# Optimization experiments

Hardware: AMD Instinct MI355X
Metric: run time of the kernel (lower is better)

The kernel has to match this reference:

```python
import jax, jax.numpy as jnp
import numpy as np
from jax import lax
from jax.scipy.special import logsumexp

B, T, N = 256, 512, 128


def setup_inputs() -> dict:
    key = jax.random.key(0)
    k1, k2, k3 = jax.random.split(key, 3)
    emissions = jax.random.normal(k1, (B, T, N), dtype=jnp.float32)
    tag_ids = jax.random.randint(k2, (B, T), 0, N, dtype=jnp.int64)
    mask = jnp.ones((B, T), dtype=jnp.int32)
    # learned transition matrix (glorot-uniform-ish init)
    limit = float(np.sqrt(6.0 / (N + N)))
    trans = jax.random.uniform(k3, (N, N), minval=-limit, maxval=limit, dtype=jnp.float32)
    return {"emissions": emissions, "tag_ids": tag_ids, "mask": mask, "trans": trans}


def _sequence_score(emissions, tag_ids, maskf, trans):
    # unary: emission score of the gold tag at each valid step
    unary = jnp.take_along_axis(emissions, tag_ids[:, :, None], axis=2)[..., 0]  # [B,T]
    unary = jnp.sum(unary * maskf, axis=1)
    # binary: transition score between consecutive gold tags
    binary = trans[tag_ids[:, :-1], tag_ids[:, 1:]] * maskf[:, 1:]  # [B,T-1]
    return unary + jnp.sum(binary, axis=1)


def _log_norm(emissions, maskf, trans):
    # forward algorithm over time via lax.scan; alpha: [B,N]
    alpha0 = emissions[:, 0]
    em = jnp.swapaxes(emissions, 0, 1)[1:]   # [T-1,B,N]
    mk = jnp.swapaxes(maskf, 0, 1)[1:]       # [T-1,B]

    def step(alpha, xs):
        emit_t, m_t = xs
        new = logsumexp(alpha[:, :, None] + trans[None], axis=1) + emit_t
        alpha = jnp.where(m_t[:, None] > 0, new, alpha)
        return alpha, None

    alpha, _ = lax.scan(step, alpha0, (em, mk))
    return logsumexp(alpha, axis=1)  # [B]


def _viterbi_decode(emissions, maskf, trans):
    alpha0 = emissions[:, 0]
    em = jnp.swapaxes(emissions, 0, 1)[1:]
    mk = jnp.swapaxes(maskf, 0, 1)[1:]
    idx = jnp.arange(N, dtype=jnp.int32)[None]

    def fwd(alpha, xs):
        emit_t, m_t = xs
        scores = alpha[:, :, None] + trans[None]        # [B,N,N]
        bp = jnp.argmax(scores, axis=1).astype(jnp.int32)  # [B,N]
        new = jnp.max(scores, axis=1) + emit_t
        valid = m_t[:, None] > 0
        alpha = jnp.where(valid, new, alpha)
        bp = jnp.where(valid, bp, idx)  # carry same tag through padding
        return alpha, bp

    alpha, bps = lax.scan(fwd, alpha0, (em, mk))  # bps: [T-1,B,N]
    last_tag = jnp.argmax(alpha, axis=1).astype(jnp.int32)  # [B]

    def bwd(tag, bp_t):
        new_tag = jnp.take_along_axis(bp_t, tag[:, None], axis=1)[:, 0]
        return new_tag, new_tag

    _, tags_rev = lax.scan(bwd, last_tag, bps[::-1])  # [T-1,B]
    tags = jnp.concatenate([tags_rev[::-1], last_tag[None]], axis=0)  # [T,B]
    return jnp.swapaxes(tags, 0, 1)  # [B,T]


def reference(emissions, tag_ids, mask, trans):
    maskf = mask.astype(emissions.dtype)
    log_likelihood = _sequence_score(emissions, tag_ids, maskf, trans) - _log_norm(emissions, maskf, trans)
    predict = _viterbi_decode(emissions, maskf, trans)
    return (log_likelihood, trans, predict)
```

## Files before the change

kernel.cpp:

```cpp
#include <hip/hip_runtime.h>
#include <cmath>

#define BB 256
#define TT 512
#define NN 128
#define LN2F 0.6931471805599453f

typedef __bf16 bf16x8 __attribute__((ext_vector_type(8)));
typedef float floatx4 __attribute__((ext_vector_type(4)));

__device__ __forceinline__ float wave_max64(float v) {
    #pragma unroll
    for (int off = 32; off; off >>= 1) v = fmaxf(v, __shfl_xor(v, off));
    return v;
}
__device__ __forceinline__ float wave_sum64(float v) {
    #pragma unroll
    for (int off = 32; off; off >>= 1) v += __shfl_xor(v, off);
    return v;
}
__device__ __forceinline__ int wave_argmax128(float v0, float v1, int l) {
    float m = fmaxf(v0, v1);
    float wm = wave_max64(m);
    unsigned long long ball = __ballot(m == wm);
    int lane = __ffsll(ball) - 1;
    int idx = (v0 == wm) ? (2 * l) : (2 * l + 1);
    return __shfl(idx, lane);
}

__device__ __forceinline__ __bf16 to_bf16(float f) {
    unsigned u = __float_as_uint(f);
    unsigned r = (u + 0x7FFFu + ((u >> 16) & 1u)) >> 16;
    union { unsigned short s; __bf16 b; } cv;
    cv.s = (unsigned short)r;
    return cv.b;
}

__device__ __forceinline__ int padidx16(int i) { return 20 * (i >> 4) + (i & 15); }

__global__ __launch_bounds__(1024, 4) void fused_kernel(
        const float* __restrict__ em, const int* __restrict__ gtags,
        const int* __restrict__ mask, const float* __restrict__ trans,
        float* __restrict__ out_ll, float* __restrict__ out_trans,
        float* __restrict__ outp) {
    const int b = blockIdx.x;
    const int tid = threadIdx.x;
    const int w = tid >> 6;
    const int l = tid & 63;
    const int jv = (l & 7) + 8 * w;
    const int q = l >> 3;
    const int i0 = 16 * q;
    const bool sAct = (w < 8);
    const int js = (l & 15) + 16 * (w & 7);
    const int qs = l >> 4;

    __shared__ __align__(16) float stA[1440], stB[1440];
    __shared__ __align__(16) __bf16 sbf[2][NN];
    __shared__ unsigned char bp_lds[TT * NN];
    __shared__ unsigned char tags_lds[TT];
    __shared__ unsigned char map_lds[16 * NN];
    __shared__ int entry_sh[16];
    __shared__ int msk[TT];
    __shared__ float piv[2];
    __shared__ float sfin[NN];
    __shared__ float wsum[16];
    __shared__ float llnorm_sh;
    __shared__ int misc[2];

    if (tid < TT) msk[tid] = mask[b * TT + tid];

    const float* emb = em + (size_t)b * TT * NN;

    float C[16];
    {
        const float* tc = trans + (size_t)i0 * NN + jv;
        #pragma unroll
        for (int r = 0; r < 16; ++r) C[r] = tc[(size_t)r * NN];
    }
    float st;
    {
        float a0 = emb[jv];
        st = a0;
        if (l < 8) stA[padidx16(jv)] = a0;
    }
    float e_next = emb[NN + jv];

    bf16x8 Bf[4];
    float ss = 0.f, es_next = 0.f;
    int kacc = 0;
    if (sAct) {
        #pragma unroll
        for (int kc = 0; kc < 4; ++kc) {
            #pragma unroll
            for (int jj = 0; jj < 8; ++jj) {
                int row = kc * 32 + qs * 8 + jj;
                Bf[kc][jj] = to_bf16(__expf(trans[(size_t)row * NN + js]));
            }
        }
        ss = __expf(emb[js]);
        if (l < 16) sbf[0][js] = to_bf16(ss);
        if (tid == 0) piv[0] = ss;
        es_next = emb[NN + js];
    }
    __syncthreads();

    const float4* apA = (const float4*)(stA + 20 * q);
    const float4* apB = (const float4*)(stB + 20 * q);

    auto STEP = [&](int t, const float4* ap, float* dst) {
        const float e_cur = e_next;
        const float es_cur = es_next;
        if (t + 1 < TT) {
            e_next = emb[(size_t)(t + 1) * NN + jv];
            if (sAct) es_next = emb[(size_t)(t + 1) * NN + js];
        }
        const int m = msk[t];
        float m0 = -INFINITY, m1 = -INFINITY, m2 = -INFINITY, m3 = -INFINITY;
        int u0 = 0, u1 = 0, u2 = 0, u3 = 0;
        #pragma unroll
        for (int u = 0; u < 4; ++u) {
            float4 v = ap[u];
            float c0 = v.x + C[4*u+0]; u0 = (c0 > m0) ? u : u0; m0 = fmaxf(m0, c0);
            float c1 = v.y + C[4*u+1]; u1 = (c1 > m1) ? u : u1; m1 = fmaxf(m1, c1);
            float c2 = v.z + C[4*u+2]; u2 = (c2 > m2) ? u : u2; m2 = fmaxf(m2, c2);
            float c3 = v.w + C[4*u+3]; u3 = (c3 > m3) ? u : u3; m3 = fmaxf(m3, c3);
        }
        float bv = m0; int bx = i0 + 4 * u0;
        { int id = i0 + 4*u1 + 1; if (m1 > bv || (m1 == bv && id < bx)) { bv = m1; bx = id; } }
        { int id = i0 + 4*u2 + 2; if (m2 > bv || (m2 == bv && id < bx)) { bv = m2; bx = id; } }
        { int id = i0 + 4*u3 + 3; if (m3 > bv || (m3 == bv && id < bx)) { bv = m3; bx = id; } }
        #pragma unroll
        for (int off = 8; off <= 32; off <<= 1) {
            float ov = __shfl_xor(bv, off);
            int oi = __shfl_xor(bx, off);
            if (ov > bv || (ov == bv && oi < bx)) { bv = ov; bx = oi; }
        }
        if (l < 8) {
            float an; int bp;
            if (m) { an = bv + e_cur; bp = bx; }
            else   { an = st;         bp = jv; }
            st = an;
            dst[padidx16(jv)] = an;
            bp_lds[t * NN + jv] = (unsigned char)bp;
        }
        if (sAct) {
            if (m) {
                const int p = (t - 1) & 1;
                const __bf16* sp = sbf[p];
                floatx4 acc = {0.f, 0.f, 0.f, 0.f};
                #pragma unroll
                for (int kc = 0; kc < 4; ++kc) {
                    bf16x8 a = *(const bf16x8*)(sp + kc * 32 + qs * 8);
                    acc = __builtin_amdgcn_mfma_f32_16x16x32_bf16(a, Bf[kc], acc, 0, 0, 0);
                }
                float dot = acc[0];
                const float pv = piv[p];
                const int k = (int)(__float_as_uint(pv) >> 23) - 127;
                const float scale = __uint_as_float((unsigned)(127 - k) << 23);
                ss = dot * scale * __expf(es_cur);
                if (tid == 0) kacc += k;
            }
            const int qb = t & 1;
            if (l < 16) sbf[qb][js] = to_bf16(ss);
            if (tid == 0) piv[qb] = ss;
        }
        __syncthreads();
    };

    for (int t = 1; t < TT - 1; t += 2) {
        STEP(t, apA, stB);
        STEP(t + 1, apB, stA);
    }
    STEP(TT - 1, apA, stB);

    if (sAct && l < 16) sfin[js] = ss;
    if (tid == 0) misc[1] = kacc;
    if (w == 0) {
        float a0 = stB[padidx16(2 * l)], a1 = stB[padidx16(2 * l + 1)];
        int tg = wave_argmax128(a0, a1, l);
        if (l == 0) { misc[0] = tg; tags_lds[TT - 1] = (unsigned char)tg; }
    }
    if (tid < 64) out_trans[b * 64 + tid] = trans[b * 64 + tid];
    __syncthreads();
    if (w == 1) {
        float v = sfin[2 * l] + sfin[2 * l + 1];
        v = wave_sum64(v);
        if (l == 0) llnorm_sh = __logf(v) + (float)misc[1] * LN2F;
    }
    const int lo = 32 * w + 1;
    const int hi = (w == 15) ? (TT - 1) : (32 * w + 32);
    {
        int tA = 2 * l, tB = 2 * l + 1;
        for (int t = hi; t >= lo; --t) {
            tA = bp_lds[t * NN + tA];
            tB = bp_lds[t * NN + tB];
        }
        map_lds[w * NN + 2 * l]     = (unsigned char)tA;
        map_lds[w * NN + 2 * l + 1] = (unsigned char)tB;
    }
    __syncthreads();
    if (tid == 0) {
        int e = misc[0];
        entry_sh[15] = e;
        for (int c = 15; c >= 1; --c) { e = map_lds[c * NN + e]; entry_sh[c - 1] = e; }
    }
    __syncthreads();
    if (l == 0) {
        int tg = entry_sh[w];
        for (int t = hi; t >= lo; --t) {
            tg = bp_lds[t * NN + tg];
            tags_lds[t - 1] = (unsigned char)tg;
        }
    }
    __syncthreads();
    float acc = 0.f;
    if (tid < TT) {
        outp[(size_t)b * TT + tid] = (float)tags_lds[tid];
        int tg = gtags[b * TT + tid];
        float mf = (float)msk[tid];
        acc = emb[(size_t)tid * NN + tg] * mf;
        if (tid >= 1) {
            int tp = gtags[b * TT + tid - 1];
            acc += trans[tp * NN + tg] * mf;
        }
    }
    acc = wave_sum64(acc);
    if (l == 0) wsum[w] = acc;
    __syncthreads();
    if (tid == 0) {
        float s = 0.f;
        #pragma unroll
        for (int i = 0; i < 16; ++i) s += wsum[i];
        out_ll[b] = s - llnorm_sh;
    }
}

extern "C" void kernel_launch(void* const* d_in, const int* in_sizes, int n_in,
                              void* d_out, int out_size, void* d_ws, size_t ws_size,
                              hipStream_t stream) {
    const float* em = (const float*)d_in[0];
    const int* gtags = (const int*)d_in[1];
    const int* mask = (const int*)d_in[2];
    const float* trans = (const float*)d_in[3];

    float* out = (float*)d_out;
    float* out_ll = out;
    float* out_trans = out + BB;
    float* out_pred = out + BB + NN * NN;

    hipLaunchKernelGGL(fused_kernel, dim3(BB), dim3(1024), 0, stream,
                       em, gtags, mask, trans, out_ll, out_trans, out_pred);
}
```

Before: 623.5 us.

## Split Viterbi and forward recurrences into separate blocks

The single fused per-batch block is split into two kinds of blocks, launched as a 2x-sized grid. The first half runs the Viterbi max-plus recurrence and backtrace, and the second half runs the MFMA-based forward log-sum-exp recurrence plus the gold-sequence score. Each block's per-step critical path and barrier work shrink, and the two chains for a sequence can run concurrently on different CUs or co-reside on one. In exchange, each block still reserves the full static shared memory, the forward block leaves half its waves idle at barriers, and emissions are read twice.

```diff
diff --git a/kernel.cpp b/kernel.cpp
--- a/kernel.cpp
+++ b/kernel.cpp
@@ -38,23 +38,19 @@
 
 __device__ __forceinline__ int padidx16(int i) { return 20 * (i >> 4) + (i & 15); }
 
-__global__ __launch_bounds__(1024, 4) void fused_kernel(
+__global__ __launch_bounds__(1024, 8) void fwd_kernel(
         const float* __restrict__ em, const int* __restrict__ gtags,
         const int* __restrict__ mask, const float* __restrict__ trans,
         float* __restrict__ out_ll, float* __restrict__ out_trans,
         float* __restrict__ outp) {
-    const int b = blockIdx.x;
+    const int bi = blockIdx.x;
+    const bool isV = bi < BB;
+    const int b = isV ? bi : bi - BB;
     const int tid = threadIdx.x;
     const int w = tid >> 6;
     const int l = tid & 63;
-    const int jv = (l & 7) + 8 * w;
-    const int q = l >> 3;
-    const int i0 = 16 * q;
-    const bool sAct = (w < 8);
-    const int js = (l & 15) + 16 * (w & 7);
-    const int qs = l >> 4;
-
-    __shared__ __align__(16) float stA[1440], stB[1440];
+
+    __shared__ __align__(16) float stA[160], stB[160];
     __shared__ __align__(16) __bf16 sbf[2][NN];
     __shared__ unsigned char bp_lds[TT * NN];
     __shared__ unsigned char tags_lds[TT];
@@ -63,7 +59,7 @@
     __shared__ int msk[TT];
     __shared__ float piv[2];
     __shared__ float sfin[NN];
-    __shared__ float wsum[16];
+    __shared__ float wsum[8];
     __shared__ float llnorm_sh;
     __shared__ int misc[2];
 
@@ -71,167 +67,182 @@
 
     const float* emb = em + (size_t)b * TT * NN;
 
-    float C[16];
-    {
-        const float* tc = trans + (size_t)i0 * NN + jv;
-        #pragma unroll
-        for (int r = 0; r < 16; ++r) C[r] = tc[(size_t)r * NN];
-    }
-    float st;
-    {
-        float a0 = emb[jv];
-        st = a0;
-        if (l < 8) stA[padidx16(jv)] = a0;
-    }
-    float e_next = emb[NN + jv];
-
-    bf16x8 Bf[4];
-    float ss = 0.f, es_next = 0.f;
-    int kacc = 0;
-    if (sAct) {
-        #pragma unroll
-        for (int kc = 0; kc < 4; ++kc) {
+    if (isV) {
+        const int jv = (l & 7) + 8 * w;
+        const int q = l >> 3;
+        const int i0 = 16 * q;
+        float4 c0, c1, c2, c3;
+        {
+            const float* tc = trans + (size_t)i0 * NN + jv;
+            #define LDC(cc, u) cc.x = tc[(4*u+0)*NN]; cc.y = tc[(4*u+1)*NN]; \
+                               cc.z = tc[(4*u+2)*NN]; cc.w = tc[(4*u+3)*NN];
+            LDC(c0, 0) LDC(c1, 1) LDC(c2, 2) LDC(c3, 3)
+            #undef LDC
+        }
+        float st;
+        {
+            float a0 = emb[jv];
+            st = a0;
+            if (l < 8) stA[padidx16(jv)] = a0;
+        }
+        float e_next = emb[NN + jv];
+        __syncthreads();
+
+        const float4* apA = (const float4*)(stA + 20 * q);
+        const float4* apB = (const float4*)(stB + 20 * q);
+
+        auto VSTEP = [&](int t, const float4* ap, float* dst) {
+            const float e_cur = e_next;
+            if (t + 1 < TT) e_next = emb[(size_t)(t + 1) * NN + jv];
+            const int m = msk[t];
+            float4 v0 = ap[0], v1 = ap[1], v2 = ap[2], v3 = ap[3];
+            float m0 = -INFINITY, m1 = -INFINITY, m2 = -INFINITY, m3 = -INFINITY;
+            int u0 = 0, u1 = 0, u2 = 0, u3 = 0;
+            #define CH(vv, cc, u) { \
+                float a = vv.x + cc.x; u0 = (a > m0) ? u : u0; m0 = fmaxf(m0, a); \
+                float bq = vv.y + cc.y; u1 = (bq > m1) ? u : u1; m1 = fmaxf(m1, bq); \
+                float c = vv.z + cc.z; u2 = (c > m2) ? u : u2; m2 = fmaxf(m2, c); \
+                float d = vv.w + cc.w; u3 = (d > m3) ? u : u3; m3 = fmaxf(m3, d); }
+            CH(v0, c0, 0) CH(v1, c1, 1) CH(v2, c2, 2) CH(v3, c3, 3)
+            #undef CH
+            float bv = m0; int bx = i0 + 4 * u0;
+            { int id = i0 + 4*u1 + 1; if (m1 > bv || (m1 == bv && id < bx)) { bv = m1; bx = id; } }
+            { int id = i0 + 4*u2 + 2; if (m2 > bv || (m2 == bv && id < bx)) { bv = m2; bx = id; } }
+            { int id = i0 + 4*u3 + 3; if (m3 > bv || (m3 == bv && id < bx)) { bv = m3; bx = id; } }
             #pragma unroll
-            for (int jj = 0; jj < 8; ++jj) {
-                int row = kc * 32 + qs * 8 + jj;
-                Bf[kc][jj] = to_bf16(__expf(trans[(size_t)row * NN + js]));
-            }
-        }
-        ss = __expf(emb[js]);
-        if (l < 16) sbf[0][js] = to_bf16(ss);
-        if (tid == 0) piv[0] = ss;
-        es_next = emb[NN + js];
-    }
-    __syncthreads();
-
-    const float4* apA = (const float4*)(stA + 20 * q);
-    const float4* apB = (const float4*)(stB + 20 * q);
-
-    auto STEP = [&](int t, const float4* ap, float* dst) {
-        const float e_cur = e_next;
-        const float es_cur = es_next;
-        if (t + 1 < TT) {
-            e_next = emb[(size_t)(t + 1) * NN + jv];
-            if (sAct) es_next = emb[(size_t)(t + 1) * NN + js];
-        }
-        const int m = msk[t];
-        float m0 = -INFINITY, m1 = -INFINITY, m2 = -INFINITY, m3 = -INFINITY;
-        int u0 = 0, u1 = 0, u2 = 0, u3 = 0;
-        #pragma unroll
-        for (int u = 0; u < 4; ++u) {
-            float4 v = ap[u];
-            float c0 = v.x + C[4*u+0]; u0 = (c0 > m0) ? u : u0; m0 = fmaxf(m0, c0);
-            float c1 = v.y + C[4*u+1]; u1 = (c1 > m1) ? u : u1; m1 = fmaxf(m1, c1);
-            float c2 = v.z + C[4*u+2]; u2 = (c2 > m2) ? u : u2; m2 = fmaxf(m2, c2);
-            float c3 = v.w + C[4*u+3]; u3 = (c3 > m3) ? u : u3; m3 = fmaxf(m3, c3);
-        }
-        float bv = m0; int bx = i0 + 4 * u0;
-        { int id = i0 + 4*u1 + 1; if (m1 > bv || (m1 == bv && id < bx)) { bv = m1; bx = id; } }
-        { int id = i0 + 4*u2 + 2; if (m2 > bv || (m2 == bv && id < bx)) { bv = m2; bx = id; } }
-        { int id = i0 + 4*u3 + 3; if (m3 > bv || (m3 == bv && id < bx)) { bv = m3; bx = id; } }
-        #pragma unroll
-        for (int off = 8; off <= 32; off <<= 1) {
-            float ov = __shfl_xor(bv, off);
-            int oi = __shfl_xor(bx, off);
-            if (ov > bv || (ov == bv && oi < bx)) { bv = ov; bx = oi; }
-        }
-        if (l < 8) {
-            float an; int bp;
-            if (m) { an = bv + e_cur; bp = bx; }
-            else   { an = st;         bp = jv; }
-            st = an;
-            dst[padidx16(jv)] = an;
-            bp_lds[t * NN + jv] = (unsigned char)bp;
-        }
+            for (int off = 8; off <= 32; off <<= 1) {
+                float ov = __shfl_xor(bv, off);
+                int oi = __shfl_xor(bx, off);
+                if (ov > bv || (ov == bv && oi < bx)) { bv = ov; bx = oi; }
+            }
+            if (l < 8) {
+                float an; int bp;
+                if (m) { an = bv + e_cur; bp = bx; }
+                else   { an = st;         bp = jv; }
+                st = an;
+                dst[padidx16(jv)] = an;
+                bp_lds[t * NN + jv] = (unsigned char)bp;
+            }
+            __syncthreads();
+        };
+
+        for (int t = 1; t < TT - 1; t += 2) {
+            VSTEP(t, apA, stB);
+            VSTEP(t + 1, apB, stA);
+        }
+        VSTEP(TT - 1, apA, stB);
+
+        if (w == 0) {
+            float a0 = stB[padidx16(2 * l)], a1 = stB[padidx16(2 * l + 1)];
+            int tg = wave_argmax128(a0, a1, l);
+            if (l == 0) { misc[0] = tg; tags_lds[TT - 1] = (unsigned char)tg; }
+        }
+        if (tid < 64) out_trans[b * 64 + tid] = trans[b * 64 + tid];
+        __syncthreads();
+        const int lo = 32 * w + 1;
+        const int hi = (w == 15) ? (TT - 1) : (32 * w + 32);
+        {
+            int tA = 2 * l, tB = 2 * l + 1;
+            for (int t = hi; t >= lo; --t) {
+                tA = bp_lds[t * NN + tA];
+                tB = bp_lds[t * NN + tB];
+            }
+            map_lds[w * NN + 2 * l]     = (unsigned char)tA;
+            map_lds[w * NN + 2 * l + 1] = (unsigned char)tB;
+        }
+        __syncthreads();
+        if (tid == 0) {
+            int e = misc[0];
+            entry_sh[15] = e;
+            for (int c = 15; c >= 1; --c) { e = map_lds[c * NN + e]; entry_sh[c - 1] = e; }
+        }
+        __syncthreads();
+        if (l == 0) {
+            int tg = entry_sh[w];
+            for (int t = hi; t >= lo; --t) {
+                tg = bp_lds[t * NN + tg];
+                tags_lds[t - 1] = (unsigned char)tg;
+            }
+        }
+        __syncthreads();
+        if (tid < TT) outp[(size_t)b * TT + tid] = (float)tags_lds[tid];
+    } else {
+        const bool sAct = (w < 8);
+        const int js = (l & 15) + 16 * w;
+        const int qs = l >> 4;
+        bf16x8 Bf[4];
+        float ss = 0.f, e_next = 0.f;
+        int kacc = 0;
         if (sAct) {
-            if (m) {
-                const int p = (t - 1) & 1;
-                const __bf16* sp = sbf[p];
-                floatx4 acc = {0.f, 0.f, 0.f, 0.f};
+            #pragma unroll
+            for (int kc = 0; kc < 4; ++kc) {
                 #pragma unroll
-                for (int kc = 0; kc < 4; ++kc) {
-                    bf16x8 a = *(const bf16x8*)(sp + kc * 32 + qs * 8);
-                    acc = __builtin_amdgcn_mfma_f32_16x16x32_bf16(a, Bf[kc], acc, 0, 0, 0);
+                for (int jj = 0; jj < 8; ++jj) {
+                    int row = kc * 32 + qs * 8 + jj;
+                    Bf[kc][jj] = to_bf16(__expf(trans[(size_t)row * NN + js]));
                 }
-                float dot = acc[0];
-                const float pv = piv[p];
-                const int k = (int)(__float_as_uint(pv) >> 23) - 127;
-                const float scale = __uint_as_float((unsigned)(127 - k) << 23);
-                ss = dot * scale * __expf(es_cur);
-                if (tid == 0) kacc += k;
-            }
-            const int qb = t & 1;
-            if (l < 16) sbf[qb][js] = to_bf16(ss);
-            if (tid == 0) piv[qb] = ss;
-        }
-        __syncthreads();
-    };
-
-    for (int t = 1; t < TT - 1; t += 2) {
-        STEP(t, apA, stB);
-        STEP(t + 1, apB, stA);
-    }
-    STEP(TT - 1, apA, stB);
-
-    if (sAct && l < 16) sfin[js] = ss;
-    if (tid == 0) misc[1] = kacc;
-    if (w == 0) {
-        float a0 = stB[padidx16(2 * l)], a1 = stB[padidx16(2 * l + 1)];
-        int tg = wave_argmax128(a0, a1, l);
-        if (l == 0) { misc[0] = tg; tags_lds[TT - 1] = (unsigned char)tg; }
-    }
-    if (tid < 64) out_trans[b * 64 + tid] = trans[b * 64 + tid];
-    __syncthreads();
-    if (w == 1) {
-        float v = sfin[2 * l] + sfin[2 * l + 1];
-        v = wave_sum64(v);
-        if (l == 0) llnorm_sh = __logf(v) + (float)misc[1] * LN2F;
-    }
-    const int lo = 32 * w + 1;
-    const int hi = (w == 15) ? (TT - 1) : (32 * w + 32);
-    {
-        int tA = 2 * l, tB = 2 * l + 1;
-        for (int t = hi; t >= lo; --t) {
-            tA = bp_lds[t * NN + tA];
-            tB = bp_lds[t * NN + tB];
-        }
-        map_lds[w * NN + 2 * l]     = (unsigned char)tA;
-        map_lds[w * NN + 2 * l + 1] = (unsigned char)tB;
-    }
-    __syncthreads();
-    if (tid == 0) {
-        int e = misc[0];
-        entry_sh[15] = e;
-        for (int c = 15; c >= 1; --c) { e = map_lds[c * NN + e]; entry_sh[c - 1] = e; }
-    }
-    __syncthreads();
-    if (l == 0) {
-        int tg = entry_sh[w];
-        for (int t = hi; t >= lo; --t) {
-            tg = bp_lds[t * NN + tg];
-            tags_lds[t - 1] = (unsigned char)tg;
-        }
-    }
-    __syncthreads();
-    float acc = 0.f;
-    if (tid < TT) {
-        outp[(size_t)b * TT + tid] = (float)tags_lds[tid];
-        int tg = gtags[b * TT + tid];
-        float mf = (float)msk[tid];
-        acc = emb[(size_t)tid * NN + tg] * mf;
-        if (tid >= 1) {
-            int tp = gtags[b * TT + tid - 1];
-            acc += trans[tp * NN + tg] * mf;
-        }
-    }
-    acc = wave_sum64(acc);
-    if (l == 0) wsum[w] = acc;
-    __syncthreads();
-    if (tid == 0) {
-        float s = 0.f;
-        #pragma unroll
-        for (int i = 0; i < 16; ++i) s += wsum[i];
-        out_ll[b] = s - llnorm_sh;
+            }
+            ss = __expf(emb[js]);
+            if (l < 16) sbf[0][js] = to_bf16(ss);
+            if (tid == 0) piv[0] = ss;
+            e_next = emb[NN + js];
+        }
+        __syncthreads();
+
+        for (int t = 1; t < TT; ++t) {
+            if (sAct) {
+                const float e_cur = e_next;
+                if (t + 1 < TT) e_next = emb[(size_t)(t + 1) * NN + js];
+                const int m = msk[t];
+                const int p = (t - 1) & 1, qb = t & 1;
+                if (m) {
+                    const __bf16* sp = sbf[p];
+                    floatx4 acc = {0.f, 0.f, 0.f, 0.f};
+                    #pragma unroll
+                    for (int kc = 0; kc < 4; ++kc) {
+                        bf16x8 a = *(const bf16x8*)(sp + kc * 32 + qs * 8);
+                        acc = __builtin_amdgcn_mfma_f32_16x16x32_bf16(a, Bf[kc], acc, 0, 0, 0);
+                    }
+                    float dot = acc[0];
+                    const float pv = piv[p];
+                    const int k = (int)(__float_as_uint(pv) >> 23) - 127;
+                    const float scale = __uint_as_float((unsigned)(127 - k) << 23);
+                    ss = dot * scale * __expf(e_cur);
+                    if (tid == 0) kacc += k;
+                }
+                if (l < 16) sbf[qb][js] = to_bf16(ss);
+                if (tid == 0) piv[qb] = ss;
+            }
+            __syncthreads();
+        }
+
+        if (sAct && l < 16) sfin[js] = ss;
+        if (tid == 0) misc[1] = kacc;
+        __syncthreads();
+        if (w == 0) {
+            float v = sfin[2 * l] + sfin[2 * l + 1];
+            v = wave_sum64(v);
+            if (l == 0) llnorm_sh = __logf(v) + (float)misc[1] * LN2F;
+        }
+        float acc = 0.f;
+        if (tid < TT) {
+            int tg = gtags[b * TT + tid];
+            float mf = (float)msk[tid];
+            acc = emb[(size_t)tid * NN + tg] * mf;
+            if (tid >= 1) {
+                int tp = gtags[b * TT + tid - 1];
+                acc += trans[tp * NN + tg] * mf;
+            }
+        }
+        acc = wave_sum64(acc);
+        if (l == 0 && w < 8) wsum[w] = acc;
+        __syncthreads();
+        if (tid == 0) {
+            float s = 0.f;
+            #pragma unroll
+            for (int i = 0; i < 8; ++i) s += wsum[i];
+            out_ll[b] = s - llnorm_sh;
+        }
     }
 }
 
@@ -248,6 +259,6 @@
     float* out_trans = out + BB;
     float* out_pred = out + BB + NN * NN;
 
-    hipLaunchKernelGGL(fused_kernel, dim3(BB), dim3(1024), 0, stream,
+    hipLaunchKernelGGL(fwd_kernel, dim3(2 * BB), dim3(1024), 0, stream,
                        em, gtags, mask, trans, out_ll, out_trans, out_pred);
 }
```

After: 586.6 us. 1.06x faster.
